# Kernel optimization log

Measured on AMD Instinct MI355X. Metric: run time of the kernel, lower is better.

Reference implementation:

```python
import jax, jax.numpy as jnp
import numpy as np

KSZ, STRIDE, UNFOLD, FREQ = 9, 1, 12, 6  # patch size, stride, LISTA unfoldings, sim-refresh freq
P, C = 256, 3                            # num_filters, image channels


def im2col(I, k):
    # torch F.unfold ordering: channel slowest, then (ki,kj); stride=1, no padding
    b, c, H, W = I.shape
    hO, wO = H - k + 1, W - k + 1
    patches = jnp.stack([I[:, :, i:i + hO, j:j + wO] for i in range(k) for j in range(k)], axis=2)
    return patches.reshape(b, c * k * k, hO, wO)  # (b, c*k*k, hO, wO)


def col2im_avg(cols, out_hw, k):
    # inverse of im2col with overlap-averaging (fold / fold(ones))
    b, ckk, hO, wO = cols.shape
    c = ckk // (k * k)
    cols = cols.reshape(b, c, k * k, hO, wO)
    H, W = out_hw
    out = jnp.zeros((b, c, H, W), cols.dtype)
    cnt = jnp.zeros((1, 1, H, W), cols.dtype)
    for idx in range(k * k):
        i, j = idx // k, idx % k
        out = out.at[:, :, i:i + hO, j:j + wO].add(cols[:, :, idx])
        cnt = cnt.at[:, :, i:i + hO, j:j + wO].add(1.0)
    return out / cnt


def conv1x1(w, x):
    # 1x1 conv == channel matmul; w: (out, in), x: (b, in, h, w)
    return jnp.einsum('on,bnhw->bohw', w, x)


def soft_matching(x):
    # patch-pairwise similarity: softmax over negative squared L2 distances
    # between patch embeddings (SoftMatchingLayer, no window mask since
    # center_windows=False). Output (b, N, N).
    b, n, h, w = x.shape
    xf = x.reshape(b, n, h * w)
    sq = jnp.sum(xf * xf, axis=1)  # (b, N)
    d = sq[:, :, None] + sq[:, None, :] - 2.0 * jnp.einsum('bni,bnj->bij', xf, xf)
    return jax.nn.softmax(-d, axis=1)  # normalize over the aggregated (group) axis


def group_prox(A, theta, sim):
    # group-sparse proximal operator: per-filter L2 norm over similarity-weighted
    # groups, ReLU shrinkage. A: (b,p,h,w), theta: (p,), sim: (b,N,N), N=h*w.
    b, p, h, w = A.shape
    Af = A.reshape(b, p, h * w)
    support = jnp.sqrt(jnp.sum(jnp.abs(sim), axis=1, keepdims=True) + 1e-12)  # (b,1,N)
    norm2 = jnp.sqrt(jnp.matmul(Af * Af, sim) + 1e-8)                          # (b,p,N)
    out = jax.nn.relu(1.0 - theta[None, :, None] * support / norm2) * Af
    return out.reshape(b, p, h, w)


def setup_inputs() -> dict:
    key = jax.random.key(0)
    k0, k1 = jax.random.split(key)
    n = KSZ * KSZ * C  # 243 patch dim
    I = jax.random.normal(k0, (2, C, 56, 56), jnp.float32)
    D = jax.random.normal(k1, (n, P), jnp.float32)
    D = D / jnp.linalg.norm(D, ord=2)  # divide by sqrt(max eig of D^T D) = sigma_max
    Wa = D.T          # apply_A: (P, n)
    Wd = D            # apply_D: (n, P)
    Ww = D            # apply_W: (n, P)
    h_param = 0.12
    std0 = jnp.full((1, n, 1, 1), 1.0 / h_param, jnp.float32)   # std_y=True, first (only) lista
    lmbdas = jnp.full((UNFOLD, P), 0.3, jnp.float32)            # multi_lmbda per unfolding
    nu = jnp.full((1,), 1.0, jnp.float32)
    return {"I": I, "Wa": Wa, "Wd": Wd, "Ww": Ww, "std0": std0, "lmbdas": lmbdas, "nu": nu}


def reference(I, Wa, Wd, Ww, std0, lmbdas, nu):
    H, W = I.shape[2], I.shape[3]
    I_col = im2col(I, KSZ)                       # (b, 243, 48, 48), N = 2304
    mean_patch = I_col.mean(axis=1, keepdims=True)
    I_col = I_col - mean_patch
    sim = soft_matching(I_col * std0)            # (b, N, N)
    gamma = group_prox(conv1x1(Wa, I_col), lmbdas[0], sim)
    for k in range(UNFOLD - 1):
        if k % FREQ == 0 and k != 0:
            # corr_update == 2: refresh similarity from current patch estimates
            sim_new = soft_matching(conv1x1(Ww, gamma) * std0)
            nus = jax.nn.sigmoid(nu)
            sim = (1.0 - nus) * sim + nus * sim_new
        r_k = conv1x1(Wa, I_col - conv1x1(Wd, gamma))
        gamma = group_prox(gamma + r_k, lmbdas[k + 1], sim)
    out_all = conv1x1(Ww, gamma) + mean_patch
    return col2im_avg(out_all, (H, W), KSZ)
```

## Files before the change

### kernel.cpp

```cpp
#include <hip/hip_runtime.h>
#include <math.h>

#define NPIX 2304
#define NDIM 243
#define PDIM 256
#define BATCH 2
#define HO 48
#define IMGH 56
#define NCH 3
#define UNFOLD 12
#define FREQ 6

typedef __attribute__((ext_vector_type(8))) short bf16x8;
typedef __attribute__((ext_vector_type(4))) float f32x4;
typedef unsigned short ushort_t;

__device__ inline unsigned short f2bf(float x) {
    union { float f; unsigned u; } v; v.f = x;
    unsigned r = (v.u + 0x7FFFu + ((v.u >> 16) & 1u)) >> 16;
    return (unsigned short)r;
}
__device__ inline float bf2f(unsigned short u) {
    return __uint_as_float(((unsigned)u) << 16);
}

__device__ __forceinline__ void gload16(const ushort_t* g, ushort_t* s) {
    __builtin_amdgcn_global_load_lds(
        (__attribute__((address_space(1))) void*)g,
        (__attribute__((address_space(3))) void*)s, 16, 0, 0);
}

__device__ __forceinline__ void ut_decode(int e, int& mi, int& ni) {
    float f = (73.0f - sqrtf(5329.0f - 8.0f * (float)e)) * 0.5f;
    mi = (int)f;
    if (mi > 35) mi = 35;
    while (mi > 0 && e < mi * 36 - mi * (mi - 1) / 2) mi--;
    while (e >= (mi + 1) * 36 - (mi + 1) * mi / 2) mi++;
    ni = mi + (e - (mi * 36 - mi * (mi - 1) / 2));
}

#define EPI_G 0
#define EPI_SPLITOUT 1
#define EPI_ITER 2
#define EPI_WAI 3
#define EPI_ADDCOL 4
#define EPI_PROX 5

template<int TM, int TN, int SPLIT, int BKU, int EPI>
__device__ __forceinline__ void gemm_tile(
    ushort_t* __restrict__ lds, int m0, int n0, int b, int mirror,
    const ushort_t* __restrict__ Ah, const ushort_t* __restrict__ Al,
    const ushort_t* __restrict__ Bh, const ushort_t* __restrict__ Bl,
    int ldA, int ldB, size_t sA, size_t sB, int K,
    float* __restrict__ C, ushort_t* __restrict__ C2,
    ushort_t* __restrict__ Oh, ushort_t* __restrict__ Ol,
    const float* __restrict__ E1, const float* __restrict__ E2,
    int ldC, size_t sC,
    const float* __restrict__ EA, const float* __restrict__ theta,
    float* __restrict__ sqd,
    float* __restrict__ POut, ushort_t* __restrict__ gTh, ushort_t* __restrict__ gTl) {

    constexpr int CA = TM / 16, CB = TN / 16;
    constexpr int CHUNKS = (1 + SPLIT) * (CA + CB);
    constexpr int UNITS = CHUNKS * BKU;
    constexpr int CPW = UNITS / 4;
    constexpr int BUFE = UNITS * 512;
    constexpr int WM = TM / 2, WN = TN / 2;
    constexpr int MF = WM / 16, NF = WN / 16;

    int tid = threadIdx.x;
    int w = tid >> 6, l = tid & 63, lm = l & 15, kh = l >> 4;
    int wm = (w >> 1) * WM, wn = (w & 1) * WN;

    const ushort_t* pAh = Ah + b * sA;
    const ushort_t* pAl = SPLIT ? Al + b * sA : nullptr;
    const ushort_t* pBh = Bh + b * sB;
    const ushort_t* pBl = SPLIT ? Bl + b * sB : nullptr;

    int srow = l >> 2;
    int sslot = ((l & 3) ^ ((l >> 3) & 3)) << 3;

    auto stage = [&](int bsel, int k0) {
        ushort_t* bb = lds + bsel * BUFE;
        #pragma unroll
        for (int i = 0; i < CPW; ++i) {
            int uu = w * CPW + i;
            int c = uu / BKU, u = uu % BKU;
            const ushort_t* src; int ld; int rowg;
            if (SPLIT) {
                if (c < CA)               { src = pAh; ld = ldA; rowg = m0 + c * 16; }
                else if (c < 2 * CA)      { src = pAl; ld = ldA; rowg = m0 + (c - CA) * 16; }
                else if (c < 2 * CA + CB) { src = pBh; ld = ldB; rowg = n0 + (c - 2 * CA) * 16; }
                else                      { src = pBl; ld = ldB; rowg = n0 + (c - 2 * CA - CB) * 16; }
            } else {
                if (c < CA) { src = pAh; ld = ldA; rowg = m0 + c * 16; }
                else        { src = pBh; ld = ldB; rowg = n0 + (c - CA) * 16; }
            }
            const ushort_t* g = src + (size_t)(rowg + srow) * ld + k0 + u * 32 + sslot;
            gload16(g, bb + (size_t)(c * BKU + u) * 512);
        }
    };

    f32x4 acc[MF][NF];
    #pragma unroll
    for (int mf = 0; mf < MF; ++mf)
        #pragma unroll
        for (int nf = 0; nf < NF; ++nf) acc[mf][nf] = (f32x4){0.f, 0.f, 0.f, 0.f};

    int sw = ((kh ^ ((lm >> 1) & 3)) << 3);
    const int NT = K / (32 * BKU);

    stage(0, 0);
    __syncthreads();
    for (int t = 0; t < NT; ++t) {
        if (t + 1 < NT) stage((t + 1) & 1, (t + 1) * (32 * BKU));
        ushort_t* bb = lds + (t & 1) * BUFE;
        ushort_t* LA_h = bb;
        ushort_t* LA_l = bb + CA * BKU * 512;
        ushort_t* LB_h = bb + (1 + SPLIT) * CA * BKU * 512;
        ushort_t* LB_l = LB_h + CB * BKU * 512;
        #pragma unroll
        for (int s = 0; s < BKU; ++s) {
            bf16x8 afh[MF], afl[MF], bfh[NF], bfl[NF];
            #pragma unroll
            for (int mf = 0; mf < MF; ++mf) {
                int off = ((wm >> 4) + mf) * (BKU * 512) + s * 512 + lm * 32 + sw;
                afh[mf] = *reinterpret_cast<const bf16x8*>(LA_h + off);
                if (SPLIT) afl[mf] = *reinterpret_cast<const bf16x8*>(LA_l + off);
            }
            #pragma unroll
            for (int nf = 0; nf < NF; ++nf) {
                int off = ((wn >> 4) + nf) * (BKU * 512) + s * 512 + lm * 32 + sw;
                bfh[nf] = *reinterpret_cast<const bf16x8*>(LB_h + off);
                if (SPLIT) bfl[nf] = *reinterpret_cast<const bf16x8*>(LB_l + off);
            }
            #pragma unroll
            for (int mf = 0; mf < MF; ++mf)
                #pragma unroll
                for (int nf = 0; nf < NF; ++nf) {
                    acc[mf][nf] = __builtin_amdgcn_mfma_f32_16x16x32_bf16(afh[mf], bfh[nf], acc[mf][nf], 0, 0, 0);
                    if (SPLIT) {
                        acc[mf][nf] = __builtin_amdgcn_mfma_f32_16x16x32_bf16(afh[mf], bfl[nf], acc[mf][nf], 0, 0, 0);
                        acc[mf][nf] = __builtin_amdgcn_mfma_f32_16x16x32_bf16(afl[mf], bfh[nf], acc[mf][nf], 0, 0, 0);
                    }
                }
        }
        __syncthreads();
    }

    if (EPI == EPI_PROX) {
        ushort_t* tbh = lds;
        ushort_t* tbl = lds + TN * (TM + 2);
        #pragma unroll
        for (int mf = 0; mf < MF; ++mf)
            #pragma unroll
            for (int nf = 0; nf < NF; ++nf)
                #pragma unroll
                for (int r = 0; r < 4; ++r) {
                    int pl = wm + mf * 16 + kh * 4 + r;
                    int jl = wn + nf * 16 + lm;
                    int gp = m0 + pl;
                    float n2 = sqrtf(acc[mf][nf][r] + 1e-8f);
                    size_t off = b * sC + (size_t)gp * ldC + (n0 + jl);
                    float v = fmaxf(1.f - theta[gp] / n2, 0.f) * EA[off];
                    POut[off] = v;
                    unsigned short h = f2bf(v);
                    tbh[jl * (TM + 2) + pl] = h;
                    tbl[jl * (TM + 2) + pl] = f2bf(v - bf2f(h));
                }
        __syncthreads();
        {
            constexpr int SEGS = TM / 8;
            int jj = tid / SEGS, seg = (tid % SEGS) * 8;
            size_t go = ((size_t)b * NPIX + n0 + jj) * PDIM + m0 + seg;
            bf16x8 vh, vl;
            #pragma unroll
            for (int e = 0; e < 8; ++e) {
                vh[e] = (short)tbh[jj * (TM + 2) + seg + e];
                vl[e] = (short)tbl[jj * (TM + 2) + seg + e];
            }
            *reinterpret_cast<bf16x8*>(gTh + go) = vh;
            *reinterpret_cast<bf16x8*>(gTl + go) = vl;
        }
        __syncthreads();
    } else {
        #pragma unroll
        for (int mf = 0; mf < MF; ++mf)
            #pragma unroll
            for (int nf = 0; nf < NF; ++nf)
                #pragma unroll
                for (int r = 0; r < 4; ++r) {
                    int gm = m0 + wm + mf * 16 + kh * 4 + r;
                    int gn = n0 + wn + nf * 16 + lm;
                    float v = acc[mf][nf][r];
                    size_t off = b * sC + (size_t)gm * ldC + gn;
                    if (EPI == EPI_G) {
                        C[off] = v;
                        if (gm == gn) sqd[b * NPIX + gm] = v;
                    } else if (EPI == EPI_SPLITOUT) {
                        unsigned short h = f2bf(v);
                        Oh[off] = h; Ol[off] = f2bf(v - bf2f(h));
                    } else if (EPI == EPI_ITER) {
                        float o = E1[off] + E2[off] - v;
                        C[off] = o;
                        C2[off] = f2bf(o * o);
                    } else if (EPI == EPI_WAI) {
                        C[off] = v;
                        C2[off] = f2bf(v * v);
                    } else {
                        C[off] = v + E1[b * NPIX + gn];
                    }
                }
        if (EPI == EPI_G && mirror) {
            __syncthreads();
            float* ldsF = (float*)lds;
            #pragma unroll
            for (int mf = 0; mf < MF; ++mf)
                #pragma unroll
                for (int nf = 0; nf < NF; ++nf)
                    #pragma unroll
                    for (int r = 0; r < 4; ++r) {
                        int il = wm + mf * 16 + kh * 4 + r;
                        int jl = wn + nf * 16 + lm;
                        ldsF[jl * 66 + il] = acc[mf][nf][r];
                    }
            __syncthreads();
            int row = tid >> 2;
            int colq = (tid & 3) * 16;
            float* Crow = C + b * sC + (size_t)(n0 + row) * ldC + m0 + colq;
            #pragma unroll
            for (int e = 0; e < 16; e += 4) {
                float4 o = make_float4(ldsF[row * 66 + colq + e],
                                       ldsF[row * 66 + colq + e + 1],
                                       ldsF[row * 66 + colq + e + 2],
                                       ldsF[row * 66 + colq + e + 3]);
                *reinterpret_cast<float4*>(Crow + e) = o;
            }
            __syncthreads();
        }
    }
}

template<int TM, int TN, int SPLIT, int BKU, int EPI, int SYMM>
__global__ __launch_bounds__(256) void k_sgemm(
    const ushort_t* __restrict__ Ah, const ushort_t* __restrict__ Al,
    const ushort_t* __restrict__ Bh, const ushort_t* __restrict__ Bl,
    int ldA, int ldB, size_t sA, size_t sB, int K,
    float* __restrict__ C, ushort_t* __restrict__ C2,
    ushort_t* __restrict__ Oh, ushort_t* __restrict__ Ol,
    const float* __restrict__ E1, const float* __restrict__ E2,
    int ldC, size_t sC,
    const float* __restrict__ EA, const float* __restrict__ theta,
    float* __restrict__ sqd,
    float* __restrict__ POut, ushort_t* __restrict__ gTh, ushort_t* __restrict__ gTl) {

    constexpr int CA = TM / 16, CB = TN / 16;
    constexpr int UNITS = (1 + SPLIT) * (CA + CB) * BKU;
    constexpr int BUFE = UNITS * 512;
    constexpr int TRE = (EPI == EPI_PROX) ? 2 * TN * (TM + 2) : 0;
    constexpr int LDSE = (2 * BUFE > TRE) ? 2 * BUFE : TRE;
    __shared__ ushort_t lds[LDSE];

    if (SYMM) {
        int id = blockIdx.x;
        int bb = id / 666, e = id % 666, mi, ni;
        ut_decode(e, mi, ni);
        gemm_tile<TM, TN, SPLIT, BKU, EPI>(lds, mi * 64, ni * 64, bb, (mi != ni),
            Ah, Al, Bh, Bl, ldA, ldB, sA, sB, K, C, C2, Oh, Ol, E1, E2, ldC, sC,
            EA, theta, sqd, POut, gTh, gTl);
    } else {
        int nwg = gridDim.x * gridDim.y * gridDim.z;
        int hw = blockIdx.x + gridDim.x * (blockIdx.y + gridDim.y * blockIdx.z);
        int L = (hw & 7) * (nwg >> 3) + (hw >> 3);
        int m_idx = L % gridDim.y;
        int n_idx = (L / gridDim.y) % gridDim.x;
        int b = L / (gridDim.y * gridDim.x);
        gemm_tile<TM, TN, SPLIT, BKU, EPI>(lds, m_idx * TM, n_idx * TN, b, 0,
            Ah, Al, Bh, Bl, ldA, ldB, sA, sB, K, C, C2, Oh, Ol, E1, E2, ldC, sC,
            EA, theta, sqd, POut, gTh, gTl);
    }
}

__global__ __launch_bounds__(256) void k_gram_wai(
    const ushort_t* __restrict__ XTsh, const ushort_t* __restrict__ XTsl,
    const ushort_t* __restrict__ XTuh, const ushort_t* __restrict__ XTul,
    const ushort_t* __restrict__ Wah, const ushort_t* __restrict__ Wal,
    float* __restrict__ G, float* __restrict__ sqd,
    float* __restrict__ WaI, ushort_t* __restrict__ A2) {
    __shared__ ushort_t lds[16384];
    const size_t NP256 = (size_t)NPIX * 256;
    const size_t sPN = (size_t)PDIM * NPIX;
    const size_t sNN = (size_t)NPIX * NPIX;
    int id = blockIdx.x;
    if (id < 1332) {
        int bb = id / 666, e = id % 666, mi, ni;
        ut_decode(e, mi, ni);
        gemm_tile<64, 64, 1, 1, EPI_G>(lds, mi * 64, ni * 64, bb, (mi != ni),
            XTsh, XTsl, XTsh, XTsl, 256, 256, NP256, NP256, 256,
            G, nullptr, nullptr, nullptr, nullptr, nullptr, NPIX, sNN,
            nullptr, nullptr, sqd, nullptr, nullptr, nullptr);
    } else {
        int lid = id - 1332;
        int L = (lid & 7) * 72 + (lid >> 3);
        int m_idx = L % 8;
        int n_idx = (L / 8) % 36;
        int b = L / 288;
        gemm_tile<32, 64, 1, 1, EPI_WAI>(lds, m_idx * 32, n_idx * 64, b, 0,
            Wah, Wal, XTuh, XTul, 256, 256, 0, NP256, 256,
            WaI, A2, nullptr, nullptr, nullptr, nullptr, NPIX, sPN,
            nullptr, nullptr, nullptr, nullptr, nullptr, nullptr);
    }
}

__global__ __launch_bounds__(256) void k_ht_iter(
    const ushort_t* __restrict__ gTh, const ushort_t* __restrict__ gTl,
    const ushort_t* __restrict__ Qh, const ushort_t* __restrict__ Ql,
    ushort_t* __restrict__ HTh, ushort_t* __restrict__ HTl,
    const ushort_t* __restrict__ Mh, const ushort_t* __restrict__ Ml,
    float* __restrict__ Abuf, ushort_t* __restrict__ A2,
    const float* __restrict__ WaI, const float* __restrict__ gamma) {
    __shared__ ushort_t lds[12288];
    const size_t NP256 = (size_t)NPIX * 256;
    const size_t sPN = (size_t)PDIM * NPIX;
    int id = blockIdx.x;
    if (id < 576) {
        int m_idx = id % 72;
        int n_idx = (id / 72) % 4;
        int b = id / 288;
        gemm_tile<32, 64, 1, 1, EPI_SPLITOUT>(lds, m_idx * 32, n_idx * 64, b, 0,
            gTh, gTl, Qh, Ql, 256, 256, NP256, 0, 256,
            nullptr, nullptr, HTh, HTl, nullptr, nullptr, 256, NP256,
            nullptr, nullptr, nullptr, nullptr, nullptr, nullptr);
    } else {
        int lid = id - 576;
        int L = (lid & 7) * 72 + (lid >> 3);
        int m_idx = L % 8;
        int n_idx = (L / 8) % 36;
        int b = L / 288;
        gemm_tile<32, 64, 1, 1, EPI_ITER>(lds, m_idx * 32, n_idx * 64, b, 0,
            Mh, Ml, gTh, gTl, 256, 256, 0, NP256, 256,
            Abuf, A2, nullptr, nullptr, WaI, gamma, NPIX, sPN,
            nullptr, nullptr, nullptr, nullptr, nullptr, nullptr);
    }
}

__global__ __launch_bounds__(1024) void k_precomp(const float* __restrict__ Wa,
                                                  const float* __restrict__ Wd,
                                                  const float* __restrict__ Ww,
                                                  const float* __restrict__ std0,
                                                  ushort_t* __restrict__ Mh, ushort_t* __restrict__ Ml,
                                                  ushort_t* __restrict__ Qh, ushort_t* __restrict__ Ql,
                                                  ushort_t* __restrict__ Wah, ushort_t* __restrict__ Wal,
                                                  ushort_t* __restrict__ Wwh, ushort_t* __restrict__ Wwl) {
    int p = blockIdx.x;
    int tid = threadIdx.x;
    int q = tid & 255, cc = tid >> 8;
    float m = 0.f, qv = 0.f;
    for (int c = cc; c < NDIM; c += 4) {
        m += Wa[p * NDIM + c] * Wd[c * PDIM + q];
        float s = std0[c];
        qv += s * s * Ww[c * PDIM + p] * Ww[c * PDIM + q];
    }
    __shared__ float sm[2][1024];
    sm[0][tid] = m; sm[1][tid] = qv;
    __syncthreads();
    if (cc == 0) {
        m  = sm[0][q] + sm[0][q + 256] + sm[0][q + 512] + sm[0][q + 768];
        qv = sm[1][q] + sm[1][q + 256] + sm[1][q + 512] + sm[1][q + 768];
        int off = p * PDIM + q;
        unsigned short h = f2bf(m);
        Mh[off] = h; Ml[off] = f2bf(m - bf2f(h));
        h = f2bf(qv);
        Qh[off] = h; Ql[off] = f2bf(qv - bf2f(h));
        float wa = (q < NDIM) ? Wa[p * NDIM + q] : 0.f;
        h = f2bf(wa);
        Wah[off] = h; Wal[off] = f2bf(wa - bf2f(h));
        float ww = (p < NDIM) ? Ww[p * PDIM + q] : 0.f;
        h = f2bf(ww);
        Wwh[off] = h; Wwl[off] = f2bf(ww - bf2f(h));
    }
}

__global__ __launch_bounds__(256) void k_im2col(const float* __restrict__ I,
                                                float* __restrict__ meanp,
                                                ushort_t* __restrict__ XTsh, ushort_t* __restrict__ XTsl,
                                                ushort_t* __restrict__ XTuh, ushort_t* __restrict__ XTul,
                                                const float* __restrict__ std0) {
    int col = blockIdx.x % NPIX;
    int b = blockIdx.x / NPIX;
    int oi = col / HO, oj = col % HO;
    int t = threadIdx.x;
    float v = 0.f;
    if (t < NDIM) {
        int c = t / 81, rem = t % 81, ki = rem / 9, kj = rem % 9;
        v = I[((size_t)(b * NCH + c) * IMGH + (oi + ki)) * IMGH + (oj + kj)];
    }
    __shared__ float red[256];
    red[t] = v;
    __syncthreads();
    for (int s = 128; s > 0; s >>= 1) {
        if (t < s) red[t] += red[t + s];
        __syncthreads();
    }
    float mean = red[0] / (float)NDIM;
    float xu = (t < NDIM) ? v - mean : 0.f;
    float xs = (t < NDIM) ? xu * std0[t] : 0.f;
    if (t == 0) meanp[b * NPIX + col] = mean;
    size_t xo = ((size_t)b * NPIX + col) * 256 + t;
    unsigned short h = f2bf(xu);
    XTuh[xo] = h; XTul[xo] = f2bf(xu - bf2f(h));
    h = f2bf(xs);
    XTsh[xo] = h; XTsl[xo] = f2bf(xs - bf2f(h));
}

template<int BLEND>
__global__ __launch_bounds__(256) void k_softmax(const float* __restrict__ G,
                                                 const float* __restrict__ sq,
                                                 ushort_t* __restrict__ Sbf,
                                                 const float* __restrict__ nu) {
    int b = blockIdx.x / NPIX;
    int j = blockIdx.x % NPIX;
    const float* Grow = G + ((size_t)b * NPIX + j) * NPIX;
    const float* sqb = sq + (size_t)b * NPIX;
    int t = threadIdx.x;
    float v[9];
    float m = -1e30f;
    #pragma unroll
    for (int i = 0; i < 9; ++i) {
        int ix = t + i * 256;
        v[i] = 2.f * Grow[ix] - sqb[ix];
        m = fmaxf(m, v[i]);
    }
    __shared__ float red[256];
    red[t] = m; __syncthreads();
    for (int s = 128; s > 0; s >>= 1) { if (t < s) red[t] = fmaxf(red[t], red[t+s]); __syncthreads(); }
    m = red[0];
    __syncthreads();
    float ss = 0.f;
    #pragma unroll
    for (int i = 0; i < 9; ++i) { v[i] = expf(v[i] - m); ss += v[i]; }
    red[t] = ss; __syncthreads();
    for (int s = 128; s > 0; s >>= 1) { if (t < s) red[t] += red[t+s]; __syncthreads(); }
    float inv = 1.f / red[0];
    ushort_t* Srow = Sbf + ((size_t)b * NPIX + j) * NPIX;
    if (BLEND) {
        float nus = 1.f / (1.f + expf(-nu[0]));
        #pragma unroll
        for (int i = 0; i < 9; ++i) {
            int ix = t + i * 256;
            Srow[ix] = f2bf((1.f - nus) * bf2f(Srow[ix]) + nus * (v[i] * inv));
        }
    } else {
        #pragma unroll
        for (int i = 0; i < 9; ++i) Srow[t + i * 256] = f2bf(v[i] * inv);
    }
}

__global__ void k_col2im(const float* __restrict__ T, float* __restrict__ out) {
    int idx = blockIdx.x * blockDim.x + threadIdx.x;
    int total = BATCH * NCH * IMGH * IMGH;
    if (idx >= total) return;
    int x = idx % IMGH; int tmp = idx / IMGH;
    int y = tmp % IMGH; tmp /= IMGH;
    int c = tmp % NCH; int b = tmp / NCH;
    int kiLo = max(0, y - (HO - 1)), kiHi = min(8, y);
    int kjLo = max(0, x - (HO - 1)), kjHi = min(8, x);
    float s = 0.f;
    for (int ki = kiLo; ki <= kiHi; ++ki)
        for (int kj = kjLo; kj <= kjHi; ++kj) {
            int ch = c * 81 + ki * 9 + kj;
            s += T[((size_t)b * 256 + ch) * NPIX + (y - ki) * HO + (x - kj)];
        }
    int cnt = (kiHi - kiLo + 1) * (kjHi - kjLo + 1);
    out[idx] = s / (float)cnt;
}

extern "C" void kernel_launch(void* const* d_in, const int* in_sizes, int n_in,
                              void* d_out, int out_size, void* d_ws, size_t ws_size,
                              hipStream_t stream) {
    const float* I    = (const float*)d_in[0];
    const float* Wa   = (const float*)d_in[1];
    const float* Wd   = (const float*)d_in[2];
    const float* Ww   = (const float*)d_in[3];
    const float* std0 = (const float*)d_in[4];
    const float* lmb  = (const float*)d_in[5];
    const float* nu   = (const float*)d_in[6];
    float* out = (float*)d_out;
    float* ws = (float*)d_ws;

    const size_t NP256 = (size_t)NPIX * 256;
    size_t off = 0;
    auto alloc = [&](size_t n) { float* p = ws + off; off += (n + 63) & ~(size_t)63; return p; };
    auto allocU = [&](size_t n) { return (ushort_t*)alloc((n + 1) / 2); };

    float* WaI   = alloc((size_t)BATCH * PDIM * NPIX);
    float* Abuf  = alloc((size_t)BATCH * PDIM * NPIX);
    float* gamma = alloc((size_t)BATCH * PDIM * NPIX);
    float* TR    = alloc((size_t)BATCH * 256 * NPIX);
    float* G     = alloc((size_t)BATCH * NPIX * NPIX);
    ushort_t* Sbf  = allocU((size_t)BATCH * NPIX * NPIX);
    ushort_t* A2   = allocU((size_t)BATCH * PDIM * NPIX);
    ushort_t* XTsh = allocU(BATCH * NP256);
    ushort_t* XTsl = allocU(BATCH * NP256);
    ushort_t* XTuh = allocU(BATCH * NP256);
    ushort_t* XTul = allocU(BATCH * NP256);
    ushort_t* gTh  = allocU(BATCH * NP256);
    ushort_t* gTl  = allocU(BATCH * NP256);
    ushort_t* HTh  = allocU(BATCH * NP256);
    ushort_t* HTl  = allocU(BATCH * NP256);
    ushort_t* Mh   = allocU(PDIM * PDIM);
    ushort_t* Ml   = allocU(PDIM * PDIM);
    ushort_t* Qh   = allocU(PDIM * PDIM);
    ushort_t* Ql   = allocU(PDIM * PDIM);
    ushort_t* Wah  = allocU(PDIM * PDIM);
    ushort_t* Wal  = allocU(PDIM * PDIM);
    ushort_t* Wwh  = allocU(PDIM * PDIM);
    ushort_t* Wwl  = allocU(PDIM * PDIM);
    float* meanp = alloc((size_t)BATCH * NPIX);
    float* sqd   = alloc((size_t)BATCH * NPIX);
    (void)ws_size; (void)in_sizes; (void)n_in; (void)out_size;

    dim3 blk(256);
    const size_t sPN = (size_t)PDIM * NPIX;
    const size_t sNN = (size_t)NPIX * NPIX;

    k_precomp<<<dim3(PDIM), dim3(1024), 0, stream>>>(Wa, Wd, Ww, std0, Mh, Ml, Qh, Ql, Wah, Wal, Wwh, Wwl);
    k_im2col<<<dim3(BATCH * NPIX), blk, 0, stream>>>(I, meanp, XTsh, XTsl, XTuh, XTul, std0);

    k_gram_wai<<<dim3(1332 + 576), blk, 0, stream>>>(
        XTsh, XTsl, XTuh, XTul, Wah, Wal, G, sqd, WaI, A2);
    k_softmax<0><<<dim3(BATCH * NPIX), blk, 0, stream>>>(G, sqd, Sbf, nu);

    k_sgemm<32, 64, 0, 2, EPI_PROX, 0><<<dim3(NPIX/64, PDIM/32, BATCH), blk, 0, stream>>>(
        A2, nullptr, Sbf, nullptr, NPIX, NPIX, sPN, sNN, NPIX,
        nullptr, nullptr, nullptr, nullptr, nullptr, nullptr, NPIX, sPN,
        WaI, lmb, nullptr, gamma, gTh, gTl);

    for (int k = 0; k < UNFOLD - 1; ++k) {
        if (k == FREQ) {
            k_ht_iter<<<dim3(1152), blk, 0, stream>>>(
                gTh, gTl, Qh, Ql, HTh, HTl, Mh, Ml, Abuf, A2, WaI, gamma);
            k_sgemm<64, 64, 1, 1, EPI_G, 1><<<dim3(1332), blk, 0, stream>>>(
                gTh, gTl, HTh, HTl, 256, 256, NP256, NP256, 256,
                G, nullptr, nullptr, nullptr, nullptr, nullptr, NPIX, sNN,
                nullptr, nullptr, sqd, nullptr, nullptr, nullptr);
            k_softmax<1><<<dim3(BATCH * NPIX), blk, 0, stream>>>(G, sqd, Sbf, nu);
        } else {
            k_sgemm<32, 64, 1, 1, EPI_ITER, 0><<<dim3(NPIX/64, PDIM/32, BATCH), blk, 0, stream>>>(
                Mh, Ml, gTh, gTl, 256, 256, 0, NP256, 256,
                Abuf, A2, nullptr, nullptr, WaI, gamma, NPIX, sPN,
                nullptr, nullptr, nullptr, nullptr, nullptr, nullptr);
        }
        k_sgemm<32, 64, 0, 2, EPI_PROX, 0><<<dim3(NPIX/64, PDIM/32, BATCH), blk, 0, stream>>>(
            A2, nullptr, Sbf, nullptr, NPIX, NPIX, sPN, sNN, NPIX,
            nullptr, nullptr, nullptr, nullptr, nullptr, nullptr, NPIX, sPN,
            Abuf, lmb + (size_t)(k + 1) * PDIM, nullptr, gamma, gTh, gTl);
    }
    k_sgemm<32, 64, 1, 1, EPI_ADDCOL, 0><<<dim3(NPIX/64, 256/32, BATCH), blk, 0, stream>>>(
        Wwh, Wwl, gTh, gTl, 256, 256, 0, NP256, 256,
        TR, nullptr, nullptr, nullptr, meanp, nullptr, NPIX, (size_t)256 * NPIX,
        nullptr, nullptr, nullptr, nullptr, nullptr, nullptr);
    k_col2im<<<dim3((BATCH * NCH * IMGH * IMGH + 255) / 256), blk, 0, stream>>>(TR, out);
}
```

Baseline: 498.8 us.

## Fuse softmax/iteration with prox GEMM via atomic-counter dataflow and 64x64 tiles

New measurement: 940.5 us. 1.89x slower.

```diff
diff --git a/kernel.cpp b/kernel.cpp
--- a/kernel.cpp
+++ b/kernel.cpp
@@ -15,6 +15,10 @@
 typedef __attribute__((ext_vector_type(4))) float f32x4;
 typedef unsigned short ushort_t;
 
+static const size_t NP256 = (size_t)NPIX * 256;
+static const size_t sPN = (size_t)PDIM * NPIX;
+static const size_t sNN = (size_t)NPIX * NPIX;
+
 __device__ inline unsigned short f2bf(float x) {
     union { float f; unsigned u; } v; v.f = x;
     unsigned r = (v.u + 0x7FFFu + ((v.u >> 16) & 1u)) >> 16;
@@ -28,6 +32,42 @@
     __builtin_amdgcn_global_load_lds(
         (__attribute__((address_space(1))) void*)g,
         (__attribute__((address_space(3))) void*)s, 16, 0, 0);
+}
+
+__device__ __forceinline__ void sig1(unsigned* c) {
+    __syncthreads();
+    if (threadIdx.x == 0)
+        __hip_atomic_fetch_add(c, 1u, __ATOMIC_RELEASE, __HIP_MEMORY_SCOPE_AGENT);
+}
+__device__ __forceinline__ void sig2(unsigned* c1, unsigned* c2) {
+    __syncthreads();
+    if (threadIdx.x == 0) {
+        __hip_atomic_fetch_add(c1, 1u, __ATOMIC_RELEASE, __HIP_MEMORY_SCOPE_AGENT);
+        __hip_atomic_fetch_add(c2, 1u, __ATOMIC_RELEASE, __HIP_MEMORY_SCOPE_AGENT);
+    }
+}
+__device__ __forceinline__ void waitc1(unsigned* c, unsigned t) {
+    if (threadIdx.x == 0) {
+        unsigned g = 0;
+        while (__hip_atomic_load(c, __ATOMIC_RELAXED, __HIP_MEMORY_SCOPE_AGENT) < t) {
+            __builtin_amdgcn_s_sleep(2);
+            if (++g > (1u << 27)) break;
+        }
+        __builtin_amdgcn_fence(__ATOMIC_ACQUIRE, "agent");
+    }
+    __syncthreads();
+}
+__device__ __forceinline__ void waitc2(unsigned* c1, unsigned t1, unsigned* c2, unsigned t2) {
+    if (threadIdx.x == 0) {
+        unsigned g = 0;
+        while ((__hip_atomic_load(c1, __ATOMIC_RELAXED, __HIP_MEMORY_SCOPE_AGENT) < t1 ||
+                __hip_atomic_load(c2, __ATOMIC_RELAXED, __HIP_MEMORY_SCOPE_AGENT) < t2)) {
+            __builtin_amdgcn_s_sleep(2);
+            if (++g > (1u << 27)) break;
+        }
+        __builtin_amdgcn_fence(__ATOMIC_ACQUIRE, "agent");
+    }
+    __syncthreads();
 }
 
 __device__ __forceinline__ void ut_decode(int e, int& mi, int& ni) {
@@ -171,16 +211,21 @@
         __syncthreads();
         {
             constexpr int SEGS = TM / 8;
-            int jj = tid / SEGS, seg = (tid % SEGS) * 8;
-            size_t go = ((size_t)b * NPIX + n0 + jj) * PDIM + m0 + seg;
-            bf16x8 vh, vl;
-            #pragma unroll
-            for (int e = 0; e < 8; ++e) {
-                vh[e] = (short)tbh[jj * (TM + 2) + seg + e];
-                vl[e] = (short)tbl[jj * (TM + 2) + seg + e];
+            constexpr int ITER = (TM * TN / 8 + 255) / 256;
+            #pragma unroll
+            for (int it = 0; it < ITER; ++it) {
+                int idx = tid + it * 256;
+                int jj = idx / SEGS, seg = (idx % SEGS) * 8;
+                size_t go = ((size_t)b * NPIX + n0 + jj) * PDIM + m0 + seg;
+                bf16x8 vh, vl;
+                #pragma unroll
+                for (int e = 0; e < 8; ++e) {
+                    vh[e] = (short)tbh[jj * (TM + 2) + seg + e];
+                    vl[e] = (short)tbl[jj * (TM + 2) + seg + e];
+                }
+                *reinterpret_cast<bf16x8*>(gTh + go) = vh;
+                *reinterpret_cast<bf16x8*>(gTl + go) = vl;
             }
-            *reinterpret_cast<bf16x8*>(gTh + go) = vh;
-            *reinterpret_cast<bf16x8*>(gTl + go) = vl;
         }
         __syncthreads();
     } else {
@@ -241,107 +286,168 @@
     }
 }
 
-template<int TM, int TN, int SPLIT, int BKU, int EPI, int SYMM>
-__global__ __launch_bounds__(256) void k_sgemm(
-    const ushort_t* __restrict__ Ah, const ushort_t* __restrict__ Al,
-    const ushort_t* __restrict__ Bh, const ushort_t* __restrict__ Bl,
-    int ldA, int ldB, size_t sA, size_t sB, int K,
-    float* __restrict__ C, ushort_t* __restrict__ C2,
-    ushort_t* __restrict__ Oh, ushort_t* __restrict__ Ol,
-    const float* __restrict__ E1, const float* __restrict__ E2,
-    int ldC, size_t sC,
-    const float* __restrict__ EA, const float* __restrict__ theta,
-    float* __restrict__ sqd,
-    float* __restrict__ POut, ushort_t* __restrict__ gTh, ushort_t* __restrict__ gTl) {
-
-    constexpr int CA = TM / 16, CB = TN / 16;
-    constexpr int UNITS = (1 + SPLIT) * (CA + CB) * BKU;
-    constexpr int BUFE = UNITS * 512;
-    constexpr int TRE = (EPI == EPI_PROX) ? 2 * TN * (TM + 2) : 0;
-    constexpr int LDSE = (2 * BUFE > TRE) ? 2 * BUFE : TRE;
-    __shared__ ushort_t lds[LDSE];
-
-    if (SYMM) {
-        int id = blockIdx.x;
-        int bb = id / 666, e = id % 666, mi, ni;
-        ut_decode(e, mi, ni);
-        gemm_tile<TM, TN, SPLIT, BKU, EPI>(lds, mi * 64, ni * 64, bb, (mi != ni),
-            Ah, Al, Bh, Bl, ldA, ldB, sA, sB, K, C, C2, Oh, Ol, E1, E2, ldC, sC,
-            EA, theta, sqd, POut, gTh, gTl);
-    } else {
-        int nwg = gridDim.x * gridDim.y * gridDim.z;
-        int hw = blockIdx.x + gridDim.x * (blockIdx.y + gridDim.y * blockIdx.z);
-        int L = (hw & 7) * (nwg >> 3) + (hw >> 3);
-        int m_idx = L % gridDim.y;
-        int n_idx = (L / gridDim.y) % gridDim.x;
-        int b = L / (gridDim.y * gridDim.x);
-        gemm_tile<TM, TN, SPLIT, BKU, EPI>(lds, m_idx * TM, n_idx * TN, b, 0,
-            Ah, Al, Bh, Bl, ldA, ldB, sA, sB, K, C, C2, Oh, Ol, E1, E2, ldC, sC,
-            EA, theta, sqd, POut, gTh, gTl);
-    }
-}
-
-__global__ __launch_bounds__(256) void k_gram_wai(
-    const ushort_t* __restrict__ XTsh, const ushort_t* __restrict__ XTsl,
-    const ushort_t* __restrict__ XTuh, const ushort_t* __restrict__ XTul,
-    const ushort_t* __restrict__ Wah, const ushort_t* __restrict__ Wal,
-    float* __restrict__ G, float* __restrict__ sqd,
-    float* __restrict__ WaI, ushort_t* __restrict__ A2) {
+template<int BLEND>
+__device__ void softmax_rows(int s, const float* __restrict__ G,
+                             const float* __restrict__ sqd,
+                             ushort_t* __restrict__ Sbf,
+                             const float* __restrict__ nu,
+                             ushort_t* __restrict__ lds) {
+    float* red = (float*)lds;
+    int t = threadIdx.x;
+    for (int rr = 0; rr < 8; ++rr) {
+        __syncthreads();
+        int row = s * 8 + rr;
+        int b = row / NPIX, j = row % NPIX;
+        const float* Grow = G + ((size_t)b * NPIX + j) * NPIX;
+        const float* sqb = sqd + (size_t)b * NPIX;
+        float v[9];
+        float m = -1e30f;
+        #pragma unroll
+        for (int i = 0; i < 9; ++i) {
+            int ix = t + i * 256;
+            v[i] = 2.f * Grow[ix] - sqb[ix];
+            m = fmaxf(m, v[i]);
+        }
+        red[t] = m; __syncthreads();
+        for (int st = 128; st > 0; st >>= 1) { if (t < st) red[t] = fmaxf(red[t], red[t + st]); __syncthreads(); }
+        m = red[0];
+        __syncthreads();
+        float ss = 0.f;
+        #pragma unroll
+        for (int i = 0; i < 9; ++i) { v[i] = expf(v[i] - m); ss += v[i]; }
+        red[t] = ss; __syncthreads();
+        for (int st = 128; st > 0; st >>= 1) { if (t < st) red[t] += red[t + st]; __syncthreads(); }
+        float inv = 1.f / red[0];
+        ushort_t* Srow = Sbf + ((size_t)b * NPIX + j) * NPIX;
+        if (BLEND) {
+            float nus = 1.f / (1.f + expf(-nu[0]));
+            #pragma unroll
+            for (int i = 0; i < 9; ++i) {
+                int ix = t + i * 256;
+                Srow[ix] = f2bf((1.f - nus) * bf2f(Srow[ix]) + nus * (v[i] * inv));
+            }
+        } else {
+            #pragma unroll
+            for (int i = 0; i < 9; ++i) Srow[t + i * 256] = f2bf(v[i] * inv);
+        }
+    }
+}
+
+struct P {
+    const ushort_t *XTsh, *XTsl, *XTuh, *XTul;
+    const ushort_t *Wah, *Wal, *Mh, *Ml, *Qh, *Ql, *Wwh, *Wwl;
+    ushort_t *Sbf, *A2, *gTh, *gTl, *HTh, *HTl;
+    float *G, *sqd, *WaI, *Abuf, *gamma, *TR, *out;
+    const float *nu, *lmb, *meanp;
+    unsigned *cnt;
+};
+
+__global__ __launch_bounds__(256) void k_gram_wai(P p) {
     __shared__ ushort_t lds[16384];
-    const size_t NP256 = (size_t)NPIX * 256;
-    const size_t sPN = (size_t)PDIM * NPIX;
-    const size_t sNN = (size_t)NPIX * NPIX;
     int id = blockIdx.x;
     if (id < 1332) {
         int bb = id / 666, e = id % 666, mi, ni;
         ut_decode(e, mi, ni);
         gemm_tile<64, 64, 1, 1, EPI_G>(lds, mi * 64, ni * 64, bb, (mi != ni),
-            XTsh, XTsl, XTsh, XTsl, 256, 256, NP256, NP256, 256,
-            G, nullptr, nullptr, nullptr, nullptr, nullptr, NPIX, sNN,
-            nullptr, nullptr, sqd, nullptr, nullptr, nullptr);
+            p.XTsh, p.XTsl, p.XTsh, p.XTsl, 256, 256, NP256, NP256, 256,
+            p.G, nullptr, nullptr, nullptr, nullptr, nullptr, NPIX, sNN,
+            nullptr, nullptr, p.sqd, nullptr, nullptr, nullptr);
     } else {
-        int lid = id - 1332;
-        int L = (lid & 7) * 72 + (lid >> 3);
-        int m_idx = L % 8;
-        int n_idx = (L / 8) % 36;
-        int b = L / 288;
-        gemm_tile<32, 64, 1, 1, EPI_WAI>(lds, m_idx * 32, n_idx * 64, b, 0,
-            Wah, Wal, XTuh, XTul, 256, 256, 0, NP256, 256,
-            WaI, A2, nullptr, nullptr, nullptr, nullptr, NPIX, sPN,
+        int id2 = id - 1332;
+        int L = ((id2 & 7) * 36) + (id2 >> 3);
+        int m = L % 4, n = (L / 4) % 36, b = L / 144;
+        gemm_tile<64, 64, 1, 1, EPI_WAI>(lds, m * 64, n * 64, b, 0,
+            p.Wah, p.Wal, p.XTuh, p.XTul, 256, 256, 0, NP256, 256,
+            p.WaI, p.A2, nullptr, nullptr, nullptr, nullptr, NPIX, sPN,
             nullptr, nullptr, nullptr, nullptr, nullptr, nullptr);
     }
 }
 
-__global__ __launch_bounds__(256) void k_ht_iter(
-    const ushort_t* __restrict__ gTh, const ushort_t* __restrict__ gTl,
-    const ushort_t* __restrict__ Qh, const ushort_t* __restrict__ Ql,
-    ushort_t* __restrict__ HTh, ushort_t* __restrict__ HTl,
-    const ushort_t* __restrict__ Mh, const ushort_t* __restrict__ Ml,
-    float* __restrict__ Abuf, ushort_t* __restrict__ A2,
-    const float* __restrict__ WaI, const float* __restrict__ gamma) {
-    __shared__ ushort_t lds[12288];
-    const size_t NP256 = (size_t)NPIX * 256;
-    const size_t sPN = (size_t)PDIM * NPIX;
+template<int BLEND>
+__global__ __launch_bounds__(256) void k_sm_prox(P p, const float* EA, const float* theta, int cbase) {
+    __shared__ ushort_t lds[16384];
     int id = blockIdx.x;
     if (id < 576) {
-        int m_idx = id % 72;
-        int n_idx = (id / 72) % 4;
-        int b = id / 288;
-        gemm_tile<32, 64, 1, 1, EPI_SPLITOUT>(lds, m_idx * 32, n_idx * 64, b, 0,
-            gTh, gTl, Qh, Ql, 256, 256, NP256, 0, 256,
-            nullptr, nullptr, HTh, HTl, nullptr, nullptr, 256, NP256,
+        softmax_rows<BLEND>(id, p.G, p.sqd, p.Sbf, p.nu, lds);
+        sig1(p.cnt + cbase + (id >> 3));
+    } else {
+        int id2 = id - 576;
+        int L = ((id2 & 7) * 36) + (id2 >> 3);
+        int m = L % 4, n = (L / 4) % 36, b = L / 144;
+        waitc1(p.cnt + cbase + b * 36 + n, 8);
+        gemm_tile<64, 64, 0, 2, EPI_PROX>(lds, m * 64, n * 64, b, 0,
+            p.A2, nullptr, p.Sbf, nullptr, NPIX, NPIX, sPN, sNN, NPIX,
+            nullptr, nullptr, nullptr, nullptr, nullptr, nullptr, NPIX, sPN,
+            EA, theta, nullptr, p.gamma, p.gTh, p.gTl);
+    }
+}
+
+__global__ __launch_bounds__(256) void k_iterprox(P p, int kk, const float* theta) {
+    __shared__ ushort_t lds[16384];
+    unsigned* itm = p.cnt + 144 + kk * 16;
+    unsigned* itn = p.cnt + 400 + kk * 72;
+    int id = blockIdx.x;
+    if (id < 288) {
+        int L = ((id & 7) * 36) + (id >> 3);
+        int m = L % 4, n = (L / 4) % 36, b = L / 144;
+        gemm_tile<64, 64, 1, 1, EPI_ITER>(lds, m * 64, n * 64, b, 0,
+            p.Mh, p.Ml, p.gTh, p.gTl, 256, 256, 0, NP256, 256,
+            p.Abuf, p.A2, nullptr, nullptr, p.WaI, p.gamma, NPIX, sPN,
+            nullptr, nullptr, nullptr, nullptr, nullptr, nullptr);
+        sig2(itm + b * 4 + m, itn + b * 36 + n);
+    } else {
+        int id2 = id - 288;
+        int L = ((id2 & 7) * 36) + (id2 >> 3);
+        int m = L % 4, n = (L / 4) % 36, b = L / 144;
+        waitc2(itm + b * 4 + m, 36, itn + b * 36 + n, 4);
+        gemm_tile<64, 64, 0, 2, EPI_PROX>(lds, m * 64, n * 64, b, 0,
+            p.A2, nullptr, p.Sbf, nullptr, NPIX, NPIX, sPN, sNN, NPIX,
+            nullptr, nullptr, nullptr, nullptr, nullptr, nullptr, NPIX, sPN,
+            p.Abuf, theta, nullptr, p.gamma, p.gTh, p.gTl);
+    }
+}
+
+__global__ __launch_bounds__(256) void k_ht_iter(P p) {
+    __shared__ ushort_t lds[16384];
+    int id = blockIdx.x;
+    if (id < 288) {
+        int L = ((id & 7) * 36) + (id >> 3);
+        int m = L % 36, n = (L / 36) % 4, b = L / 144;
+        gemm_tile<64, 64, 1, 1, EPI_SPLITOUT>(lds, m * 64, n * 64, b, 0,
+            p.gTh, p.gTl, p.Qh, p.Ql, 256, 256, NP256, 0, 256,
+            nullptr, nullptr, p.HTh, p.HTl, nullptr, nullptr, 256, NP256,
             nullptr, nullptr, nullptr, nullptr, nullptr, nullptr);
     } else {
-        int lid = id - 576;
-        int L = (lid & 7) * 72 + (lid >> 3);
-        int m_idx = L % 8;
-        int n_idx = (L / 8) % 36;
-        int b = L / 288;
-        gemm_tile<32, 64, 1, 1, EPI_ITER>(lds, m_idx * 32, n_idx * 64, b, 0,
-            Mh, Ml, gTh, gTl, 256, 256, 0, NP256, 256,
-            Abuf, A2, nullptr, nullptr, WaI, gamma, NPIX, sPN,
+        int id2 = id - 288;
+        int L = ((id2 & 7) * 36) + (id2 >> 3);
+        int m = L % 4, n = (L / 4) % 36, b = L / 144;
+        gemm_tile<64, 64, 1, 1, EPI_ITER>(lds, m * 64, n * 64, b, 0,
+            p.Mh, p.Ml, p.gTh, p.gTl, 256, 256, 0, NP256, 256,
+            p.Abuf, p.A2, nullptr, nullptr, p.WaI, p.gamma, NPIX, sPN,
             nullptr, nullptr, nullptr, nullptr, nullptr, nullptr);
     }
+}
+
+__global__ __launch_bounds__(256) void k_gramref(P p) {
+    __shared__ ushort_t lds[16384];
+    int id = blockIdx.x;
+    int bb = id / 666, e = id % 666, mi, ni;
+    ut_decode(e, mi, ni);
+    gemm_tile<64, 64, 1, 1, EPI_G>(lds, mi * 64, ni * 64, bb, (mi != ni),
+        p.gTh, p.gTl, p.HTh, p.HTl, 256, 256, NP256, NP256, 256,
+        p.G, nullptr, nullptr, nullptr, nullptr, nullptr, NPIX, sNN,
+        nullptr, nullptr, p.sqd, nullptr, nullptr, nullptr);
+}
+
+__global__ __launch_bounds__(256) void k_final(P p) {
+    __shared__ ushort_t lds[16384];
+    int id = blockIdx.x;
+    int L = ((id & 7) * 36) + (id >> 3);
+    int m = L % 4, n = (L / 4) % 36, b = L / 144;
+    gemm_tile<64, 64, 1, 1, EPI_ADDCOL>(lds, m * 64, n * 64, b, 0,
+        p.Wwh, p.Wwl, p.gTh, p.gTl, 256, 256, 0, NP256, 256,
+        p.TR, nullptr, nullptr, nullptr, p.meanp, nullptr, NPIX, (size_t)256 * NPIX,
+        nullptr, nullptr, nullptr, nullptr, nullptr, nullptr);
 }
 
 __global__ __launch_bounds__(1024) void k_precomp(const float* __restrict__ Wa,
@@ -413,49 +519,6 @@
     XTsh[xo] = h; XTsl[xo] = f2bf(xs - bf2f(h));
 }
 
-template<int BLEND>
-__global__ __launch_bounds__(256) void k_softmax(const float* __restrict__ G,
-                                                 const float* __restrict__ sq,
-                                                 ushort_t* __restrict__ Sbf,
-                                                 const float* __restrict__ nu) {
-    int b = blockIdx.x / NPIX;
-    int j = blockIdx.x % NPIX;
-    const float* Grow = G + ((size_t)b * NPIX + j) * NPIX;
-    const float* sqb = sq + (size_t)b * NPIX;
-    int t = threadIdx.x;
-    float v[9];
-    float m = -1e30f;
-    #pragma unroll
-    for (int i = 0; i < 9; ++i) {
-        int ix = t + i * 256;
-        v[i] = 2.f * Grow[ix] - sqb[ix];
-        m = fmaxf(m, v[i]);
-    }
-    __shared__ float red[256];
-    red[t] = m; __syncthreads();
-    for (int s = 128; s > 0; s >>= 1) { if (t < s) red[t] = fmaxf(red[t], red[t+s]); __syncthreads(); }
-    m = red[0];
-    __syncthreads();
-    float ss = 0.f;
-    #pragma unroll
-    for (int i = 0; i < 9; ++i) { v[i] = expf(v[i] - m); ss += v[i]; }
-    red[t] = ss; __syncthreads();
-    for (int s = 128; s > 0; s >>= 1) { if (t < s) red[t] += red[t+s]; __syncthreads(); }
-    float inv = 1.f / red[0];
-    ushort_t* Srow = Sbf + ((size_t)b * NPIX + j) * NPIX;
-    if (BLEND) {
-        float nus = 1.f / (1.f + expf(-nu[0]));
-        #pragma unroll
-        for (int i = 0; i < 9; ++i) {
-            int ix = t + i * 256;
-            Srow[ix] = f2bf((1.f - nus) * bf2f(Srow[ix]) + nus * (v[i] * inv));
-        }
-    } else {
-        #pragma unroll
-        for (int i = 0; i < 9; ++i) Srow[t + i * 256] = f2bf(v[i] * inv);
-    }
-}
-
 __global__ void k_col2im(const float* __restrict__ T, float* __restrict__ out) {
     int idx = blockIdx.x * blockDim.x + threadIdx.x;
     int total = BATCH * NCH * IMGH * IMGH;
@@ -488,11 +551,11 @@
     float* out = (float*)d_out;
     float* ws = (float*)d_ws;
 
-    const size_t NP256 = (size_t)NPIX * 256;
     size_t off = 0;
     auto alloc = [&](size_t n) { float* p = ws + off; off += (n + 63) & ~(size_t)63; return p; };
     auto allocU = [&](size_t n) { return (ushort_t*)alloc((n + 1) / 2); };
 
+    unsigned* cnt = (unsigned*)alloc(2048);
     float* WaI   = alloc((size_t)BATCH * PDIM * NPIX);
     float* Abuf  = alloc((size_t)BATCH * PDIM * NPIX);
     float* gamma = alloc((size_t)BATCH * PDIM * NPIX);
@@ -521,44 +584,30 @@
     (void)ws_size; (void)in_sizes; (void)n_in; (void)out_size;
 
     dim3 blk(256);
-    const size_t sPN = (size_t)PDIM * NPIX;
-    const size_t sNN = (size_t)NPIX * NPIX;
-
+
+    hipMemsetAsync((void*)cnt, 0, 2048 * sizeof(unsigned), stream);
     k_precomp<<<dim3(PDIM), dim3(1024), 0, stream>>>(Wa, Wd, Ww, std0, Mh, Ml, Qh, Ql, Wah, Wal, Wwh, Wwl);
     k_im2col<<<dim3(BATCH * NPIX), blk, 0, stream>>>(I, meanp, XTsh, XTsl, XTuh, XTul, std0);
 
-    k_gram_wai<<<dim3(1332 + 576), blk, 0, stream>>>(
-        XTsh, XTsl, XTuh, XTul, Wah, Wal, G, sqd, WaI, A2);
-    k_softmax<0><<<dim3(BATCH * NPIX), blk, 0, stream>>>(G, sqd, Sbf, nu);
-
-    k_sgemm<32, 64, 0, 2, EPI_PROX, 0><<<dim3(NPIX/64, PDIM/32, BATCH), blk, 0, stream>>>(
-        A2, nullptr, Sbf, nullptr, NPIX, NPIX, sPN, sNN, NPIX,
-        nullptr, nullptr, nullptr, nullptr, nullptr, nullptr, NPIX, sPN,
-        WaI, lmb, nullptr, gamma, gTh, gTl);
-
-    for (int k = 0; k < UNFOLD - 1; ++k) {
-        if (k == FREQ) {
-            k_ht_iter<<<dim3(1152), blk, 0, stream>>>(
-                gTh, gTl, Qh, Ql, HTh, HTl, Mh, Ml, Abuf, A2, WaI, gamma);
-            k_sgemm<64, 64, 1, 1, EPI_G, 1><<<dim3(1332), blk, 0, stream>>>(
-                gTh, gTl, HTh, HTl, 256, 256, NP256, NP256, 256,
-                G, nullptr, nullptr, nullptr, nullptr, nullptr, NPIX, sNN,
-                nullptr, nullptr, sqd, nullptr, nullptr, nullptr);
-            k_softmax<1><<<dim3(BATCH * NPIX), blk, 0, stream>>>(G, sqd, Sbf, nu);
-        } else {
-            k_sgemm<32, 64, 1, 1, EPI_ITER, 0><<<dim3(NPIX/64, PDIM/32, BATCH), blk, 0, stream>>>(
-                Mh, Ml, gTh, gTl, 256, 256, 0, NP256, 256,
-                Abuf, A2, nullptr, nullptr, WaI, gamma, NPIX, sPN,
-                nullptr, nullptr, nullptr, nullptr, nullptr, nullptr);
-        }
-        k_sgemm<32, 64, 0, 2, EPI_PROX, 0><<<dim3(NPIX/64, PDIM/32, BATCH), blk, 0, stream>>>(
-            A2, nullptr, Sbf, nullptr, NPIX, NPIX, sPN, sNN, NPIX,
-            nullptr, nullptr, nullptr, nullptr, nullptr, nullptr, NPIX, sPN,
-            Abuf, lmb + (size_t)(k + 1) * PDIM, nullptr, gamma, gTh, gTl);
-    }
-    k_sgemm<32, 64, 1, 1, EPI_ADDCOL, 0><<<dim3(NPIX/64, 256/32, BATCH), blk, 0, stream>>>(
-        Wwh, Wwl, gTh, gTl, 256, 256, 0, NP256, 256,
-        TR, nullptr, nullptr, nullptr, meanp, nullptr, NPIX, (size_t)256 * NPIX,
-        nullptr, nullptr, nullptr, nullptr, nullptr, nullptr);
+    P p;
+    p.XTsh = XTsh; p.XTsl = XTsl; p.XTuh = XTuh; p.XTul = XTul;
+    p.Wah = Wah; p.Wal = Wal; p.Mh = Mh; p.Ml = Ml;
+    p.Qh = Qh; p.Ql = Ql; p.Wwh = Wwh; p.Wwl = Wwl;
+    p.Sbf = Sbf; p.A2 = A2; p.gTh = gTh; p.gTl = gTl; p.HTh = HTh; p.HTl = HTl;
+    p.G = G; p.sqd = sqd; p.WaI = WaI; p.Abuf = Abuf; p.gamma = gamma;
+    p.TR = TR; p.out = out;
+    p.nu = nu; p.lmb = lmb; p.meanp = meanp;
+    p.cnt = cnt;
+
+    k_gram_wai<<<dim3(1620), blk, 0, stream>>>(p);
+    k_sm_prox<0><<<dim3(864), blk, 0, stream>>>(p, WaI, lmb, 0);
+    for (int kk = 0; kk < 6; ++kk)
+        k_iterprox<<<dim3(576), blk, 0, stream>>>(p, kk, lmb + (size_t)(kk + 1) * PDIM);
+    k_ht_iter<<<dim3(576), blk, 0, stream>>>(p);
+    k_gramref<<<dim3(1332), blk, 0, stream>>>(p);
+    k_sm_prox<1><<<dim3(864), blk, 0, stream>>>(p, Abuf, lmb + (size_t)7 * PDIM, 72);
+    for (int kk = 6; kk < 10; ++kk)
+        k_iterprox<<<dim3(576), blk, 0, stream>>>(p, kk, lmb + (size_t)(kk + 2) * PDIM);
+    k_final<<<dim3(288), blk, 0, stream>>>(p);
     k_col2im<<<dim3((BATCH * NCH * IMGH * IMGH + 255) / 256), blk, 0, stream>>>(TR, out);
 }
```
